# Optimization experiments

Hardware: AMD Instinct MI355X
Metric: run time of the kernel (lower is better)

The kernel has to match this reference:

```python
import jax, jax.numpy as jnp
import numpy as np

B, L, E, H = 1024, 50, 256, 256
NEG = -1e9          # stands in for -inf masked_fill (exp(NEG) == 0 in fp32)
C_EXPL = 10.0       # tanh_exploration for the pointer head
N_GLIMPSES = 1


def setup_inputs() -> dict:
    key = jax.random.key(0)
    ks = jax.random.split(key, 20)
    s = 1.0 / np.sqrt(H).astype(np.float32)
    return {
        "decoder_input": jax.random.normal(ks[0], (B, E), jnp.float32),
        "embedded_inputs": jax.random.normal(ks[1], (L, B, E), jnp.float32),
        "h0": jax.random.normal(ks[2], (B, H), jnp.float32),
        "c0": jax.random.normal(ks[3], (B, H), jnp.float32),
        "context": jax.random.normal(ks[4], (L, B, H), jnp.float32),
        "init_mask": jnp.zeros((B, L), dtype=bool),
        "lstm_Wih": jax.random.normal(ks[5], (4 * H, E), jnp.float32) * s,
        "lstm_Whh": jax.random.normal(ks[6], (4 * H, H), jnp.float32) * s,
        "lstm_bih": jax.random.normal(ks[7], (4 * H,), jnp.float32) * s,
        "lstm_bhh": jax.random.normal(ks[8], (4 * H,), jnp.float32) * s,
        "gl_Wq": jax.random.normal(ks[9], (H, H), jnp.float32) * s,
        "gl_bq": jax.random.normal(ks[10], (H,), jnp.float32) * s,
        "gl_Wref": jax.random.normal(ks[11], (H, H), jnp.float32) * s,
        "gl_bref": jax.random.normal(ks[12], (H,), jnp.float32) * s,
        "gl_v": jax.random.uniform(ks[13], (H,), jnp.float32, -s, s),
        "pt_Wq": jax.random.normal(ks[14], (H, H), jnp.float32) * s,
        "pt_bq": jax.random.normal(ks[15], (H, H // H * H,)[:1] and (H,), jnp.float32) * s,
        "pt_Wref": jax.random.normal(ks[16], (H, H), jnp.float32) * s,
        "pt_bref": jax.random.normal(ks[17], (H,), jnp.float32) * s,
        "pt_v": jax.random.uniform(ks[18], (H,), jnp.float32, -s, s),
    }


def _attention(Wq, bq, Wref, bref, v, query, context, use_tanh):
    # context: [L,B,H], query: [B,H]
    e = jnp.einsum('lbh,oh->lbo', context, Wref) + bref      # conv1d(k=1) proj of ref
    q = query @ Wq.T + bq                                    # [B,H]
    u = jnp.einsum('lbh,h->bl', jnp.tanh(q[None, :, :] + e), v)
    if use_tanh:
        u = C_EXPL * jnp.tanh(u)
    return e, u


def _lstm_cell(x, h, c, Wih, Whh, bih, bhh):
    g = x @ Wih.T + bih + h @ Whh.T + bhh
    i, f, gg, o = jnp.split(g, 4, axis=1)   # torch LSTMCell gate order: i,f,g,o
    c2 = jax.nn.sigmoid(f) * c + jax.nn.sigmoid(i) * jnp.tanh(gg)
    h2 = jax.nn.sigmoid(o) * jnp.tanh(c2)
    return h2, c2


def reference(decoder_input, embedded_inputs, h0, c0, context, init_mask,
              lstm_Wih, lstm_Whh, lstm_bih, lstm_bhh,
              gl_Wq, gl_bq, gl_Wref, gl_bref, gl_v,
              pt_Wq, pt_bq, pt_Wref, pt_bref, pt_v):
    batch_idx = jnp.arange(B)

    def step(carry, t):
        h, c, mask, idxs, dec_in = carry
        # update_mask(mask, selected), skipped at step 0 (prev_idxs is None)
        safe = jnp.maximum(idxs, 0)
        m2 = mask.at[batch_idx, safe].set(True)
        m2 = m2.at[:, -1].set(jnp.where(m2.all(axis=1), False, m2[:, -1]))
        logit_mask = jnp.where(t == 0, mask, m2)
        # LSTM cell
        hy, cy = _lstm_cell(dec_in, h, c, lstm_Wih, lstm_Whh, lstm_bih, lstm_bhh)
        g_l = hy
        # glimpse attention(s) (mask_glimpses=True)
        for _ in range(N_GLIMPSES):
            e, gl = _attention(gl_Wq, gl_bq, gl_Wref, gl_bref, gl_v, g_l, context, False)
            gl = jnp.where(logit_mask, NEG, gl)
            g_l = jnp.einsum('lbh,bl->bh', e, jax.nn.softmax(gl, axis=1))
        # pointer attention (mask_logits=True)
        _, logits = _attention(pt_Wq, pt_bq, pt_Wref, pt_bref, pt_v, g_l, context, True)
        logits = jnp.where(logit_mask, NEG, logits)
        log_p = jax.nn.log_softmax(logits, axis=1)          # [B,L]
        new_idxs = jax.lax.stop_gradient(jnp.argmax(log_p, axis=1))  # greedy decode (detached)
        new_dec_in = embedded_inputs[new_idxs, batch_idx]   # gather next input [B,E]
        return (hy, cy, logit_mask, new_idxs, new_dec_in), (log_p, new_idxs)

    init = (h0, c0, init_mask, jnp.full((B,), -1, dtype=jnp.int32), decoder_input)
    _, (log_ps, sels) = jax.lax.scan(step, init, jnp.arange(L))
    # stack along time dim 1, as torch.stack(outputs, 1)
    return jnp.transpose(log_ps, (1, 0, 2)), jnp.transpose(sels, (1, 0))
```

## Files before the change

kernel.cpp:

```cpp
#include <hip/hip_runtime.h>
#include <math.h>

#define Bsz 1024
#define Lsz 50
#define Esz 256
#define Hsz 256
#define NEGV (-1e9f)

__global__ void init_kernel(const float* __restrict__ dec0,
                            float* __restrict__ dec,
                            int* __restrict__ mask)
{
    int i = blockIdx.x * 256 + threadIdx.x;
    dec[i] = dec0[i];
    if (i < Bsz * Lsz) mask[i] = 0;
}

__global__ void transpose_wq(const float* __restrict__ WqGl, const float* __restrict__ WqPt,
                             float* __restrict__ WqGlT, float* __restrict__ WqPtT)
{
    int k = blockIdx.x;
    int n = threadIdx.x;
    if (blockIdx.y == 0) WqGlT[k * 256 + n] = WqGl[n * 256 + k];
    else                 WqPtT[k * 256 + n] = WqPt[n * 256 + k];
}

__global__ __launch_bounds__(256) void eproj_kernel(const float* __restrict__ A,
                                                    const float* __restrict__ W,
                                                    const float* __restrict__ bias,
                                                    float* __restrict__ Eo)
{
    __shared__ __align__(16) float As[16][64];
    __shared__ __align__(16) float Bs[16][64];
    const int tid = threadIdx.x;
    const int tx = tid & 15, ty = tid >> 4;
    const int ml = tid >> 2;
    const int kb = (tid & 3) << 2;
    const int m0 = blockIdx.x * 64, n0 = blockIdx.y * 64;
    const int K = Hsz;
    float acc[4][4] = {};
    for (int k0 = 0; k0 < K; k0 += 16) {
        float4 a4 = *(const float4*)(A + (size_t)(m0 + ml) * K + k0 + kb);
        float4 b4 = *(const float4*)(W + (size_t)(n0 + ml) * K + k0 + kb);
        As[kb+0][ml] = a4.x; As[kb+1][ml] = a4.y; As[kb+2][ml] = a4.z; As[kb+3][ml] = a4.w;
        Bs[kb+0][ml] = b4.x; Bs[kb+1][ml] = b4.y; Bs[kb+2][ml] = b4.z; Bs[kb+3][ml] = b4.w;
        __syncthreads();
#pragma unroll
        for (int kk = 0; kk < 16; kk++) {
            float4 av = *(const float4*)(&As[kk][ty << 2]);
            float4 bv = *(const float4*)(&Bs[kk][tx << 2]);
            float a_[4] = {av.x, av.y, av.z, av.w};
            float b_[4] = {bv.x, bv.y, bv.z, bv.w};
#pragma unroll
            for (int i = 0; i < 4; i++)
#pragma unroll
                for (int j = 0; j < 4; j++) acc[i][j] = fmaf(a_[i], b_[j], acc[i][j]);
        }
        __syncthreads();
    }
#pragma unroll
    for (int i = 0; i < 4; i++) {
        int m = m0 + (ty << 2) + i;
        int bb = m & (Bsz - 1);
        int ll = m >> 10;
#pragma unroll
        for (int j = 0; j < 4; j++) {
            int n = n0 + (tx << 2) + j;
            Eo[(size_t)bb * Lsz * Hsz + (size_t)ll * Hsz + n] = acc[i][j] + bias[n];
        }
    }
}

__global__ __launch_bounds__(256) void lstm_fused(
    const float* __restrict__ dec, const float* __restrict__ hprev,
    const float* __restrict__ cin,
    const float* __restrict__ Wih, const float* __restrict__ Whh,
    const float* __restrict__ bih, const float* __restrict__ bhh,
    float* __restrict__ hout, float* __restrict__ cout)
{
    __shared__ __align__(16) float As[16][64];
    __shared__ __align__(16) float Bs[16][64];
    const int tid = threadIdx.x;
    const int tx = tid & 15, ty = tid >> 4;
    const int ml = tid >> 2;
    const int kb = (tid & 3) << 2;
    const int m0 = blockIdx.x * 64;
    const int hh0 = blockIdx.y * 16;
    const int wrow = ((ml >> 4) << 8) + hh0 + (ml & 15);
    const int pcol = ((ml & 15) << 2) + (ml >> 4);

    float4 a4 = *(const float4*)(dec + (size_t)(m0 + ml) * 256 + kb);
    float4 b4 = *(const float4*)(Wih + (size_t)wrow * 256 + kb);

    float acc[4][4] = {};
    for (int k0 = 0; k0 < 512; k0 += 16) {
        As[kb+0][ml] = a4.x; As[kb+1][ml] = a4.y; As[kb+2][ml] = a4.z; As[kb+3][ml] = a4.w;
        Bs[kb+0][pcol] = b4.x; Bs[kb+1][pcol] = b4.y; Bs[kb+2][pcol] = b4.z; Bs[kb+3][pcol] = b4.w;
        __syncthreads();
        int k1 = k0 + 16;
        if (k1 < 512) {
            const float* A = (k1 < 256) ? dec : hprev;
            const float* W = (k1 < 256) ? Wih : Whh;
            int kk0 = k1 & 255;
            a4 = *(const float4*)(A + (size_t)(m0 + ml) * 256 + kk0 + kb);
            b4 = *(const float4*)(W + (size_t)wrow * 256 + kk0 + kb);
        }
#pragma unroll
        for (int kk = 0; kk < 16; kk++) {
            float4 av = *(const float4*)(&As[kk][ty << 2]);
            float4 bv = *(const float4*)(&Bs[kk][tx << 2]);
            float a_[4] = {av.x, av.y, av.z, av.w};
            float b_[4] = {bv.x, bv.y, bv.z, bv.w};
#pragma unroll
            for (int i = 0; i < 4; i++)
#pragma unroll
                for (int j = 0; j < 4; j++) acc[i][j] = fmaf(a_[i], b_[j], acc[i][j]);
        }
        __syncthreads();
    }

    const int hh = hh0 + tx;
    const float bi0 = bih[hh]       + bhh[hh];
    const float bf  = bih[256 + hh] + bhh[256 + hh];
    const float bg  = bih[512 + hh] + bhh[512 + hh];
    const float bo  = bih[768 + hh] + bhh[768 + hh];
#pragma unroll
    for (int i = 0; i < 4; i++) {
        int m = m0 + (ty << 2) + i;
        float gi = acc[i][0] + bi0;
        float gf = acc[i][1] + bf;
        float gc = acc[i][2] + bg;
        float go = acc[i][3] + bo;
        float ii = 1.0f / (1.0f + expf(-gi));
        float ff = 1.0f / (1.0f + expf(-gf));
        float oo = 1.0f / (1.0f + expf(-go));
        float c2 = ff * cin[(size_t)m * 256 + hh] + ii * tanhf(gc);
        hout[(size_t)m * 256 + hh] = oo * tanhf(c2);
        cout[(size_t)m * 256 + hh] = c2;
    }
}

template<bool PTR>
__global__ __launch_bounds__(256) void attn_kernel(
    const float* __restrict__ hq, const float* __restrict__ WqT,
    const float* __restrict__ bq,
    const float* __restrict__ e, const float* __restrict__ v,
    int* __restrict__ mask,
    float* __restrict__ g_out, float* __restrict__ out, int t,
    float* __restrict__ dec, const float* __restrict__ emb)
{
    __shared__ float h_s[256];
    __shared__ __align__(16) float q_s[256];
    __shared__ float u_s[64];
    __shared__ float p_s[64];
    __shared__ int sel_s;

    const int tid = threadIdx.x;
    const int lane = tid & 63, wave = tid >> 6;
    const int b = blockIdx.x;

    h_s[tid] = hq[(size_t)b * 256 + tid];
    __syncthreads();

    float q = bq[tid];
#pragma unroll 8
    for (int k = 0; k < 256; k++)
        q = fmaf(h_s[k], WqT[(size_t)k * 256 + tid], q);
    q_s[tid] = q;
    __syncthreads();

    const float4 q4 = ((const float4*)q_s)[lane];
    const float4 v4 = ((const float4*)v)[lane];
    const float* eb = e + (size_t)b * Lsz * 256;

#pragma unroll
    for (int lp = 0; lp < 13; lp++) {
        const int l = lp * 4 + wave;
        float x = 0.0f;
        if (l < Lsz) {
            float4 e4 = *(const float4*)(eb + (size_t)l * 256 + (lane << 2));
            x = v4.x * tanhf(q4.x + e4.x);
            x += v4.y * tanhf(q4.y + e4.y);
            x += v4.z * tanhf(q4.z + e4.z);
            x += v4.w * tanhf(q4.w + e4.w);
        }
#pragma unroll
        for (int o = 32; o > 0; o >>= 1) x += __shfl_xor(x, o, 64);
        if (lane == 0 && l < Lsz) u_s[l] = x;
    }
    __syncthreads();

    if (wave == 0) {
        const int l = lane;
        const int ml = (l < Lsz) ? mask[b * Lsz + l] : 0;
        float logit;
        if (l < Lsz) {
            float u = u_s[l];
            logit = PTR ? 10.0f * tanhf(u) : u;
            if (ml) logit = NEGV;
        } else logit = -1e30f;

        float m = logit;
#pragma unroll
        for (int o = 32; o > 0; o >>= 1) m = fmaxf(m, __shfl_xor(m, o, 64));
        float ex = (l < Lsz) ? expf(logit - m) : 0.0f;
        float den = ex;
#pragma unroll
        for (int o = 32; o > 0; o >>= 1) den += __shfl_xor(den, o, 64);

        if (!PTR) {
            if (l < Lsz) p_s[l] = ex / den;
        } else {
            float av = logit; int ai = (l < Lsz) ? l : 63;
#pragma unroll
            for (int o = 32; o > 0; o >>= 1) {
                float ov = __shfl_xor(av, o, 64);
                int   oi = __shfl_xor(ai, o, 64);
                if (ov > av || (ov == av && oi < ai)) { av = ov; ai = oi; }
            }
            const float lse = m + logf(den);
            if (l < Lsz)
                out[(size_t)b * Lsz * Lsz + (size_t)t * Lsz + l] = logit - lse;
            if (l == 0) {
                out[(size_t)Bsz * Lsz * Lsz + (size_t)b * Lsz + t] = (float)ai;
                sel_s = ai;
            }
            int newm = ml | (l == ai);
            unsigned long long bal = __ballot(l >= Lsz ? 1 : newm);
            int all = (bal == 0xFFFFFFFFFFFFFFFFull);
            if (l < Lsz) mask[b * Lsz + l] = (all && l == Lsz - 1) ? 0 : newm;
        }
    }
    __syncthreads();

    if (!PTR) {
        float acc = 0.0f;
        const float* ebh = eb + tid;
#pragma unroll
        for (int l = 0; l < Lsz; l++)
            acc = fmaf(p_s[l], ebh[(size_t)l * 256], acc);
        g_out[(size_t)b * 256 + tid] = acc;
    } else {
        const int s = sel_s;
        dec[(size_t)b * 256 + tid] = emb[(size_t)s * Bsz * 256 + (size_t)b * 256 + tid];
    }
}

extern "C" void kernel_launch(void* const* d_in, const int* in_sizes, int n_in,
                              void* d_out, int out_size, void* d_ws, size_t ws_size,
                              hipStream_t stream) {
    const float* decoder_input = (const float*)d_in[0];
    const float* emb           = (const float*)d_in[1];
    const float* h0            = (const float*)d_in[2];
    const float* c0            = (const float*)d_in[3];
    const float* context       = (const float*)d_in[4];
    const float* Wih    = (const float*)d_in[6];
    const float* Whh    = (const float*)d_in[7];
    const float* bih    = (const float*)d_in[8];
    const float* bhh    = (const float*)d_in[9];
    const float* glWq   = (const float*)d_in[10];
    const float* glbq   = (const float*)d_in[11];
    const float* glWref = (const float*)d_in[12];
    const float* glbref = (const float*)d_in[13];
    const float* glv    = (const float*)d_in[14];
    const float* ptWq   = (const float*)d_in[15];
    const float* ptbq   = (const float*)d_in[16];
    const float* ptWref = (const float*)d_in[17];
    const float* ptbref = (const float*)d_in[18];
    const float* ptv    = (const float*)d_in[19];

    float* out = (float*)d_out;

    float* ws    = (float*)d_ws;
    float* e_gl  = ws;
    float* e_pt  = e_gl + (size_t)Bsz * Lsz * Hsz;
    float* WqGlT = e_pt + (size_t)Bsz * Lsz * Hsz;
    float* WqPtT = WqGlT + (size_t)Hsz * Hsz;
    float* hb0   = WqPtT + (size_t)Hsz * Hsz;
    float* hb1   = hb0 + (size_t)Bsz * Hsz;
    float* cb0   = hb1 + (size_t)Bsz * Hsz;
    float* cb1   = cb0 + (size_t)Bsz * Hsz;
    float* gb    = cb1 + (size_t)Bsz * Hsz;
    float* dec   = gb  + (size_t)Bsz * Hsz;
    int*   mask  = (int*)(dec + (size_t)Bsz * Esz);

    float* hbuf[2] = {hb0, hb1};
    float* cbuf[2] = {cb0, cb1};

    init_kernel<<<dim3(Bsz), dim3(256), 0, stream>>>(decoder_input, dec, mask);
    transpose_wq<<<dim3(256, 2), dim3(256), 0, stream>>>(glWq, ptWq, WqGlT, WqPtT);

    dim3 ge(Lsz * Bsz / 64, Hsz / 64);
    eproj_kernel<<<ge, dim3(256), 0, stream>>>(context, glWref, glbref, e_gl);
    eproj_kernel<<<ge, dim3(256), 0, stream>>>(context, ptWref, ptbref, e_pt);

    for (int t = 0; t < Lsz; t++) {
        const float* hin = (t == 0) ? h0 : hbuf[(t + 1) & 1];
        const float* cin = (t == 0) ? c0 : cbuf[(t + 1) & 1];
        float* hout = hbuf[t & 1];
        float* cout = cbuf[t & 1];

        lstm_fused<<<dim3(16, 16), dim3(256), 0, stream>>>(
            dec, hin, cin, Wih, Whh, bih, bhh, hout, cout);

        attn_kernel<false><<<dim3(Bsz), dim3(256), 0, stream>>>(
            hout, WqGlT, glbq, e_gl, glv, mask, gb, nullptr, t, nullptr, nullptr);

        attn_kernel<true><<<dim3(Bsz), dim3(256), 0, stream>>>(
            gb, WqPtT, ptbq, e_pt, ptv, mask, nullptr, out, t, dec, emb);
    }
}
```

Before: 4.579 ms.

## Fuse glimpse and pointer attention into one kernel, two batch rows per block

The separate glimpse and pointer attention kernels are merged into one kernel per step. Each block now handles two batch rows, so every Wq weight load is reused for two query projections, and the glimpse result stays in shared memory instead of going through a global buffer. The shared-memory tiles in the GEMM kernels are padded from 64 to 68 columns to reduce bank conflicts, and the eproj grid is reordered so that the N-tiles of the same rows run next to each other. The cost is half as many blocks per launch (512), which lowers parallelism, and more sequential work per block.

New measurement: 5.369 ms. 17.2% more time.

```diff
diff --git a/kernel.cpp b/kernel.cpp
--- a/kernel.cpp
+++ b/kernel.cpp
@@ -30,13 +30,13 @@
                                                     const float* __restrict__ bias,
                                                     float* __restrict__ Eo)
 {
-    __shared__ __align__(16) float As[16][64];
-    __shared__ __align__(16) float Bs[16][64];
+    __shared__ __align__(16) float As[16][68];
+    __shared__ __align__(16) float Bs[16][68];
     const int tid = threadIdx.x;
     const int tx = tid & 15, ty = tid >> 4;
     const int ml = tid >> 2;
     const int kb = (tid & 3) << 2;
-    const int m0 = blockIdx.x * 64, n0 = blockIdx.y * 64;
+    const int n0 = blockIdx.x * 64, m0 = blockIdx.y * 64;
     const int K = Hsz;
     float acc[4][4] = {};
     for (int k0 = 0; k0 < K; k0 += 16) {
@@ -78,8 +78,8 @@
     const float* __restrict__ bih, const float* __restrict__ bhh,
     float* __restrict__ hout, float* __restrict__ cout)
 {
-    __shared__ __align__(16) float As[16][64];
-    __shared__ __align__(16) float Bs[16][64];
+    __shared__ __align__(16) float As[16][68];
+    __shared__ __align__(16) float Bs[16][68];
     const int tid = threadIdx.x;
     const int tx = tid & 15, ty = tid >> 4;
     const int ml = tid >> 2;
@@ -140,63 +140,132 @@
     }
 }
 
-template<bool PTR>
-__global__ __launch_bounds__(256) void attn_kernel(
-    const float* __restrict__ hq, const float* __restrict__ WqT,
-    const float* __restrict__ bq,
-    const float* __restrict__ e, const float* __restrict__ v,
-    int* __restrict__ mask,
-    float* __restrict__ g_out, float* __restrict__ out, int t,
+__global__ __launch_bounds__(256) void attn_fused(
+    const float* __restrict__ h,
+    const float* __restrict__ WqGlT, const float* __restrict__ glbq,
+    const float* __restrict__ e_gl, const float* __restrict__ glv,
+    const float* __restrict__ WqPtT, const float* __restrict__ ptbq,
+    const float* __restrict__ e_pt, const float* __restrict__ ptv,
+    int* __restrict__ mask, float* __restrict__ out, int t,
     float* __restrict__ dec, const float* __restrict__ emb)
 {
-    __shared__ float h_s[256];
-    __shared__ __align__(16) float q_s[256];
-    __shared__ float u_s[64];
-    __shared__ float p_s[64];
-    __shared__ int sel_s;
+    __shared__ float h2[2][256];
+    __shared__ __align__(16) float q_s[2][256];
+    __shared__ float g2[2][256];
+    __shared__ float u_s[2][64];
+    __shared__ float p_s[2][64];
+    __shared__ int   sel_s[2];
 
     const int tid = threadIdx.x;
     const int lane = tid & 63, wave = tid >> 6;
-    const int b = blockIdx.x;
-
-    h_s[tid] = hq[(size_t)b * 256 + tid];
-    __syncthreads();
-
-    float q = bq[tid];
+    const int b0 = blockIdx.x * 2;
+
+    h2[0][tid] = h[(size_t)b0 * 256 + tid];
+    h2[1][tid] = h[(size_t)(b0 + 1) * 256 + tid];
+    __syncthreads();
+
+    float q0 = glbq[tid], q1 = q0;
 #pragma unroll 8
-    for (int k = 0; k < 256; k++)
-        q = fmaf(h_s[k], WqT[(size_t)k * 256 + tid], q);
-    q_s[tid] = q;
-    __syncthreads();
-
-    const float4 q4 = ((const float4*)q_s)[lane];
-    const float4 v4 = ((const float4*)v)[lane];
-    const float* eb = e + (size_t)b * Lsz * 256;
-
-#pragma unroll
-    for (int lp = 0; lp < 13; lp++) {
-        const int l = lp * 4 + wave;
-        float x = 0.0f;
-        if (l < Lsz) {
-            float4 e4 = *(const float4*)(eb + (size_t)l * 256 + (lane << 2));
-            x = v4.x * tanhf(q4.x + e4.x);
-            x += v4.y * tanhf(q4.y + e4.y);
-            x += v4.z * tanhf(q4.z + e4.z);
-            x += v4.w * tanhf(q4.w + e4.w);
-        }
-#pragma unroll
-        for (int o = 32; o > 0; o >>= 1) x += __shfl_xor(x, o, 64);
-        if (lane == 0 && l < Lsz) u_s[l] = x;
-    }
-    __syncthreads();
-
-    if (wave == 0) {
-        const int l = lane;
+    for (int k = 0; k < 256; k++) {
+        float w = WqGlT[(size_t)k * 256 + tid];
+        q0 = fmaf(h2[0][k], w, q0);
+        q1 = fmaf(h2[1][k], w, q1);
+    }
+    q_s[0][tid] = q0; q_s[1][tid] = q1;
+    __syncthreads();
+
+    const float4 vg4 = ((const float4*)glv)[lane];
+
+#pragma unroll
+    for (int r = 0; r < 2; r++) {
+        const float4 q4 = ((const float4*)q_s[r])[lane];
+        const float* eb = e_gl + (size_t)(b0 + r) * Lsz * 256;
+#pragma unroll
+        for (int lp = 0; lp < 13; lp++) {
+            const int l = lp * 4 + wave;
+            float x = 0.0f;
+            if (l < Lsz) {
+                float4 e4 = *(const float4*)(eb + (size_t)l * 256 + (lane << 2));
+                x  = vg4.x * tanhf(q4.x + e4.x);
+                x += vg4.y * tanhf(q4.y + e4.y);
+                x += vg4.z * tanhf(q4.z + e4.z);
+                x += vg4.w * tanhf(q4.w + e4.w);
+            }
+#pragma unroll
+            for (int o = 32; o > 0; o >>= 1) x += __shfl_xor(x, o, 64);
+            if (lane == 0 && l < Lsz) u_s[r][l] = x;
+        }
+    }
+    __syncthreads();
+
+    if (wave < 2) {
+        const int r = wave, l = lane;
+        const int ml = (l < Lsz) ? mask[(b0 + r) * Lsz + l] : 0;
+        float logit = (l < Lsz) ? (ml ? NEGV : u_s[r][l]) : -1e30f;
+        float m = logit;
+#pragma unroll
+        for (int o = 32; o > 0; o >>= 1) m = fmaxf(m, __shfl_xor(m, o, 64));
+        float ex = (l < Lsz) ? expf(logit - m) : 0.0f;
+        float den = ex;
+#pragma unroll
+        for (int o = 32; o > 0; o >>= 1) den += __shfl_xor(den, o, 64);
+        if (l < Lsz) p_s[r][l] = ex / den;
+    }
+    __syncthreads();
+
+#pragma unroll
+    for (int r = 0; r < 2; r++) {
+        const float* ebh = e_gl + (size_t)(b0 + r) * Lsz * 256 + tid;
+        float acc = 0.0f;
+#pragma unroll
+        for (int l = 0; l < Lsz; l++)
+            acc = fmaf(p_s[r][l], ebh[(size_t)l * 256], acc);
+        g2[r][tid] = acc;
+    }
+    __syncthreads();
+
+    float p0 = ptbq[tid], p1 = p0;
+#pragma unroll 8
+    for (int k = 0; k < 256; k++) {
+        float w = WqPtT[(size_t)k * 256 + tid];
+        p0 = fmaf(g2[0][k], w, p0);
+        p1 = fmaf(g2[1][k], w, p1);
+    }
+    q_s[0][tid] = p0; q_s[1][tid] = p1;
+    __syncthreads();
+
+    const float4 vp4 = ((const float4*)ptv)[lane];
+
+#pragma unroll
+    for (int r = 0; r < 2; r++) {
+        const float4 q4 = ((const float4*)q_s[r])[lane];
+        const float* eb = e_pt + (size_t)(b0 + r) * Lsz * 256;
+#pragma unroll
+        for (int lp = 0; lp < 13; lp++) {
+            const int l = lp * 4 + wave;
+            float x = 0.0f;
+            if (l < Lsz) {
+                float4 e4 = *(const float4*)(eb + (size_t)l * 256 + (lane << 2));
+                x  = vp4.x * tanhf(q4.x + e4.x);
+                x += vp4.y * tanhf(q4.y + e4.y);
+                x += vp4.z * tanhf(q4.z + e4.z);
+                x += vp4.w * tanhf(q4.w + e4.w);
+            }
+#pragma unroll
+            for (int o = 32; o > 0; o >>= 1) x += __shfl_xor(x, o, 64);
+            if (lane == 0 && l < Lsz) u_s[r][l] = x;
+        }
+    }
+    __syncthreads();
+
+    if (wave < 2) {
+        const int r = wave, l = lane;
+        const int b = b0 + r;
         const int ml = (l < Lsz) ? mask[b * Lsz + l] : 0;
         float logit;
         if (l < Lsz) {
-            float u = u_s[l];
-            logit = PTR ? 10.0f * tanhf(u) : u;
+            float u = u_s[r][l];
+            logit = 10.0f * tanhf(u);
             if (ml) logit = NEGV;
         } else logit = -1e30f;
 
@@ -208,41 +277,32 @@
 #pragma unroll
         for (int o = 32; o > 0; o >>= 1) den += __shfl_xor(den, o, 64);
 
-        if (!PTR) {
-            if (l < Lsz) p_s[l] = ex / den;
-        } else {
-            float av = logit; int ai = (l < Lsz) ? l : 63;
-#pragma unroll
-            for (int o = 32; o > 0; o >>= 1) {
-                float ov = __shfl_xor(av, o, 64);
-                int   oi = __shfl_xor(ai, o, 64);
-                if (ov > av || (ov == av && oi < ai)) { av = ov; ai = oi; }
-            }
-            const float lse = m + logf(den);
-            if (l < Lsz)
-                out[(size_t)b * Lsz * Lsz + (size_t)t * Lsz + l] = logit - lse;
-            if (l == 0) {
-                out[(size_t)Bsz * Lsz * Lsz + (size_t)b * Lsz + t] = (float)ai;
-                sel_s = ai;
-            }
-            int newm = ml | (l == ai);
-            unsigned long long bal = __ballot(l >= Lsz ? 1 : newm);
-            int all = (bal == 0xFFFFFFFFFFFFFFFFull);
-            if (l < Lsz) mask[b * Lsz + l] = (all && l == Lsz - 1) ? 0 : newm;
-        }
-    }
-    __syncthreads();
-
-    if (!PTR) {
-        float acc = 0.0f;
-        const float* ebh = eb + tid;
-#pragma unroll
-        for (int l = 0; l < Lsz; l++)
-            acc = fmaf(p_s[l], ebh[(size_t)l * 256], acc);
-        g_out[(size_t)b * 256 + tid] = acc;
-    } else {
-        const int s = sel_s;
-        dec[(size_t)b * 256 + tid] = emb[(size_t)s * Bsz * 256 + (size_t)b * 256 + tid];
+        float av = logit; int ai = (l < Lsz) ? l : 63;
+#pragma unroll
+        for (int o = 32; o > 0; o >>= 1) {
+            float ov = __shfl_xor(av, o, 64);
+            int   oi = __shfl_xor(ai, o, 64);
+            if (ov > av || (ov == av && oi < ai)) { av = ov; ai = oi; }
+        }
+        const float lse = m + logf(den);
+        if (l < Lsz)
+            out[(size_t)b * Lsz * Lsz + (size_t)t * Lsz + l] = logit - lse;
+        if (l == 0) {
+            out[(size_t)Bsz * Lsz * Lsz + (size_t)b * Lsz + t] = (float)ai;
+            sel_s[r] = ai;
+        }
+        int newm = ml | (l == ai);
+        unsigned long long bal = __ballot(l >= Lsz ? 1 : newm);
+        int all = (bal == 0xFFFFFFFFFFFFFFFFull);
+        if (l < Lsz) mask[b * Lsz + l] = (all && l == Lsz - 1) ? 0 : newm;
+    }
+    __syncthreads();
+
+#pragma unroll
+    for (int r = 0; r < 2; r++) {
+        const int s = sel_s[r];
+        dec[(size_t)(b0 + r) * 256 + tid] =
+            emb[(size_t)s * Bsz * 256 + (size_t)(b0 + r) * 256 + tid];
     }
 }
 
@@ -280,8 +340,7 @@
     float* hb1   = hb0 + (size_t)Bsz * Hsz;
     float* cb0   = hb1 + (size_t)Bsz * Hsz;
     float* cb1   = cb0 + (size_t)Bsz * Hsz;
-    float* gb    = cb1 + (size_t)Bsz * Hsz;
-    float* dec   = gb  + (size_t)Bsz * Hsz;
+    float* dec   = cb1 + (size_t)Bsz * Hsz;
     int*   mask  = (int*)(dec + (size_t)Bsz * Esz);
 
     float* hbuf[2] = {hb0, hb1};
@@ -290,7 +349,7 @@
     init_kernel<<<dim3(Bsz), dim3(256), 0, stream>>>(decoder_input, dec, mask);
     transpose_wq<<<dim3(256, 2), dim3(256), 0, stream>>>(glWq, ptWq, WqGlT, WqPtT);
 
-    dim3 ge(Lsz * Bsz / 64, Hsz / 64);
+    dim3 ge(Hsz / 64, Lsz * Bsz / 64);
     eproj_kernel<<<ge, dim3(256), 0, stream>>>(context, glWref, glbref, e_gl);
     eproj_kernel<<<ge, dim3(256), 0, stream>>>(context, ptWref, ptbref, e_pt);
 
@@ -303,10 +362,8 @@
         lstm_fused<<<dim3(16, 16), dim3(256), 0, stream>>>(
             dec, hin, cin, Wih, Whh, bih, bhh, hout, cout);
 
-        attn_kernel<false><<<dim3(Bsz), dim3(256), 0, stream>>>(
-            hout, WqGlT, glbq, e_gl, glv, mask, gb, nullptr, t, nullptr, nullptr);
-
-        attn_kernel<true><<<dim3(Bsz), dim3(256), 0, stream>>>(
-            gb, WqPtT, ptbq, e_pt, ptv, mask, nullptr, out, t, dec, emb);
-    }
-}
+        attn_fused<<<dim3(512), dim3(256), 0, stream>>>(
+            hout, WqGlT, glbq, e_gl, glv, WqPtT, ptbq, e_pt, ptv,
+            mask, out, t, dec, emb);
+    }
+}
```

## Fuse glimpse and pointer attention into one per-row kernel; pad LDS and remap eproj tiles

Applied to the files above, without the earlier changes.

Merges the glimpse and pointer attention kernels into a single per-batch-row kernel. The glimpse vector now stays in shared memory instead of going through a global buffer, and each step needs one fewer launch. The eproj kernel gets a 1D grid with an XCD-aware tile remap so that the N-tiles of the same M-tile land on the same chiplet and share its L2. Both GEMM kernels pad their shared tiles from 64 to 68 columns to reduce bank conflicts. The fused kernel does more serial work per block, which may lengthen per-block latency.

Measured after the change: 4.383 ms. -4.3%, faster.

```diff
diff --git a/kernel.cpp b/kernel.cpp
--- a/kernel.cpp
+++ b/kernel.cpp
@@ -30,13 +30,20 @@
                                                     const float* __restrict__ bias,
                                                     float* __restrict__ Eo)
 {
-    __shared__ __align__(16) float As[16][64];
-    __shared__ __align__(16) float Bs[16][64];
+    __shared__ __align__(16) float As[16][68];
+    __shared__ __align__(16) float Bs[16][68];
     const int tid = threadIdx.x;
     const int tx = tid & 15, ty = tid >> 4;
     const int ml = tid >> 2;
     const int kb = (tid & 3) << 2;
-    const int m0 = blockIdx.x * 64, n0 = blockIdx.y * 64;
+
+    const int x = blockIdx.x;
+    const int xcd = x & 7;
+    const int j = x >> 3;
+    const int mt = xcd * 100 + (j >> 2);
+    const int nt = j & 3;
+    const int m0 = mt * 64, n0 = nt * 64;
+
     const int K = Hsz;
     float acc[4][4] = {};
     for (int k0 = 0; k0 < K; k0 += 16) {
@@ -54,7 +61,7 @@
 #pragma unroll
             for (int i = 0; i < 4; i++)
 #pragma unroll
-                for (int j = 0; j < 4; j++) acc[i][j] = fmaf(a_[i], b_[j], acc[i][j]);
+                for (int j2 = 0; j2 < 4; j2++) acc[i][j2] = fmaf(a_[i], b_[j2], acc[i][j2]);
         }
         __syncthreads();
     }
@@ -64,9 +71,9 @@
         int bb = m & (Bsz - 1);
         int ll = m >> 10;
 #pragma unroll
-        for (int j = 0; j < 4; j++) {
-            int n = n0 + (tx << 2) + j;
-            Eo[(size_t)bb * Lsz * Hsz + (size_t)ll * Hsz + n] = acc[i][j] + bias[n];
+        for (int j2 = 0; j2 < 4; j2++) {
+            int n = n0 + (tx << 2) + j2;
+            Eo[(size_t)bb * Lsz * Hsz + (size_t)ll * Hsz + n] = acc[i][j2] + bias[n];
         }
     }
 }
@@ -78,8 +85,8 @@
     const float* __restrict__ bih, const float* __restrict__ bhh,
     float* __restrict__ hout, float* __restrict__ cout)
 {
-    __shared__ __align__(16) float As[16][64];
-    __shared__ __align__(16) float Bs[16][64];
+    __shared__ __align__(16) float As[16][68];
+    __shared__ __align__(16) float Bs[16][68];
     const int tid = threadIdx.x;
     const int tx = tid & 15, ty = tid >> 4;
     const int ml = tid >> 2;
@@ -140,17 +147,18 @@
     }
 }
 
-template<bool PTR>
-__global__ __launch_bounds__(256) void attn_kernel(
-    const float* __restrict__ hq, const float* __restrict__ WqT,
-    const float* __restrict__ bq,
-    const float* __restrict__ e, const float* __restrict__ v,
-    int* __restrict__ mask,
-    float* __restrict__ g_out, float* __restrict__ out, int t,
+__global__ __launch_bounds__(256) void attn_row(
+    const float* __restrict__ h,
+    const float* __restrict__ WqGlT, const float* __restrict__ glbq,
+    const float* __restrict__ e_gl, const float* __restrict__ glv,
+    const float* __restrict__ WqPtT, const float* __restrict__ ptbq,
+    const float* __restrict__ e_pt, const float* __restrict__ ptv,
+    int* __restrict__ mask, float* __restrict__ out, int t,
     float* __restrict__ dec, const float* __restrict__ emb)
 {
     __shared__ float h_s[256];
     __shared__ __align__(16) float q_s[256];
+    __shared__ float g_s[256];
     __shared__ float u_s[64];
     __shared__ float p_s[64];
     __shared__ int sel_s;
@@ -159,34 +167,89 @@
     const int lane = tid & 63, wave = tid >> 6;
     const int b = blockIdx.x;
 
-    h_s[tid] = hq[(size_t)b * 256 + tid];
-    __syncthreads();
-
-    float q = bq[tid];
+    h_s[tid] = h[(size_t)b * 256 + tid];
+    __syncthreads();
+
+    float q = glbq[tid];
 #pragma unroll 8
     for (int k = 0; k < 256; k++)
-        q = fmaf(h_s[k], WqT[(size_t)k * 256 + tid], q);
+        q = fmaf(h_s[k], WqGlT[(size_t)k * 256 + tid], q);
     q_s[tid] = q;
     __syncthreads();
 
-    const float4 q4 = ((const float4*)q_s)[lane];
-    const float4 v4 = ((const float4*)v)[lane];
-    const float* eb = e + (size_t)b * Lsz * 256;
-
-#pragma unroll
-    for (int lp = 0; lp < 13; lp++) {
-        const int l = lp * 4 + wave;
-        float x = 0.0f;
-        if (l < Lsz) {
-            float4 e4 = *(const float4*)(eb + (size_t)l * 256 + (lane << 2));
-            x = v4.x * tanhf(q4.x + e4.x);
-            x += v4.y * tanhf(q4.y + e4.y);
-            x += v4.z * tanhf(q4.z + e4.z);
-            x += v4.w * tanhf(q4.w + e4.w);
-        }
-#pragma unroll
-        for (int o = 32; o > 0; o >>= 1) x += __shfl_xor(x, o, 64);
-        if (lane == 0 && l < Lsz) u_s[l] = x;
+    const float* ebg = e_gl + (size_t)b * Lsz * 256;
+    {
+        const float4 q4 = ((const float4*)q_s)[lane];
+        const float4 v4 = ((const float4*)glv)[lane];
+#pragma unroll
+        for (int lp = 0; lp < 13; lp++) {
+            const int l = lp * 4 + wave;
+            float x = 0.0f;
+            if (l < Lsz) {
+                float4 e4 = *(const float4*)(ebg + (size_t)l * 256 + (lane << 2));
+                x  = v4.x * tanhf(q4.x + e4.x);
+                x += v4.y * tanhf(q4.y + e4.y);
+                x += v4.z * tanhf(q4.z + e4.z);
+                x += v4.w * tanhf(q4.w + e4.w);
+            }
+#pragma unroll
+            for (int o = 32; o > 0; o >>= 1) x += __shfl_xor(x, o, 64);
+            if (lane == 0 && l < Lsz) u_s[l] = x;
+        }
+    }
+    __syncthreads();
+
+    if (wave == 0) {
+        const int l = lane;
+        const int ml = (l < Lsz) ? mask[b * Lsz + l] : 0;
+        float logit = (l < Lsz) ? (ml ? NEGV : u_s[l]) : -1e30f;
+        float m = logit;
+#pragma unroll
+        for (int o = 32; o > 0; o >>= 1) m = fmaxf(m, __shfl_xor(m, o, 64));
+        float ex = (l < Lsz) ? expf(logit - m) : 0.0f;
+        float den = ex;
+#pragma unroll
+        for (int o = 32; o > 0; o >>= 1) den += __shfl_xor(den, o, 64);
+        if (l < Lsz) p_s[l] = ex / den;
+    }
+    __syncthreads();
+
+    {
+        float acc = 0.0f;
+        const float* ebh = ebg + tid;
+#pragma unroll
+        for (int l = 0; l < Lsz; l++)
+            acc = fmaf(p_s[l], ebh[(size_t)l * 256], acc);
+        g_s[tid] = acc;
+    }
+    __syncthreads();
+
+    float p = ptbq[tid];
+#pragma unroll 8
+    for (int k = 0; k < 256; k++)
+        p = fmaf(g_s[k], WqPtT[(size_t)k * 256 + tid], p);
+    q_s[tid] = p;
+    __syncthreads();
+
+    const float* ebp = e_pt + (size_t)b * Lsz * 256;
+    {
+        const float4 q4 = ((const float4*)q_s)[lane];
+        const float4 v4 = ((const float4*)ptv)[lane];
+#pragma unroll
+        for (int lp = 0; lp < 13; lp++) {
+            const int l = lp * 4 + wave;
+            float x = 0.0f;
+            if (l < Lsz) {
+                float4 e4 = *(const float4*)(ebp + (size_t)l * 256 + (lane << 2));
+                x  = v4.x * tanhf(q4.x + e4.x);
+                x += v4.y * tanhf(q4.y + e4.y);
+                x += v4.z * tanhf(q4.z + e4.z);
+                x += v4.w * tanhf(q4.w + e4.w);
+            }
+#pragma unroll
+            for (int o = 32; o > 0; o >>= 1) x += __shfl_xor(x, o, 64);
+            if (lane == 0 && l < Lsz) u_s[l] = x;
+        }
     }
     __syncthreads();
 
@@ -196,7 +259,7 @@
         float logit;
         if (l < Lsz) {
             float u = u_s[l];
-            logit = PTR ? 10.0f * tanhf(u) : u;
+            logit = 10.0f * tanhf(u);
             if (ml) logit = NEGV;
         } else logit = -1e30f;
 
@@ -208,39 +271,28 @@
 #pragma unroll
         for (int o = 32; o > 0; o >>= 1) den += __shfl_xor(den, o, 64);
 
-        if (!PTR) {
-            if (l < Lsz) p_s[l] = ex / den;
-        } else {
-            float av = logit; int ai = (l < Lsz) ? l : 63;
-#pragma unroll
-            for (int o = 32; o > 0; o >>= 1) {
-                float ov = __shfl_xor(av, o, 64);
-                int   oi = __shfl_xor(ai, o, 64);
-                if (ov > av || (ov == av && oi < ai)) { av = ov; ai = oi; }
-            }
-            const float lse = m + logf(den);
-            if (l < Lsz)
-                out[(size_t)b * Lsz * Lsz + (size_t)t * Lsz + l] = logit - lse;
-            if (l == 0) {
-                out[(size_t)Bsz * Lsz * Lsz + (size_t)b * Lsz + t] = (float)ai;
-                sel_s = ai;
-            }
-            int newm = ml | (l == ai);
-            unsigned long long bal = __ballot(l >= Lsz ? 1 : newm);
-            int all = (bal == 0xFFFFFFFFFFFFFFFFull);
-            if (l < Lsz) mask[b * Lsz + l] = (all && l == Lsz - 1) ? 0 : newm;
-        }
-    }
-    __syncthreads();
-
-    if (!PTR) {
-        float acc = 0.0f;
-        const float* ebh = eb + tid;
-#pragma unroll
-        for (int l = 0; l < Lsz; l++)
-            acc = fmaf(p_s[l], ebh[(size_t)l * 256], acc);
-        g_out[(size_t)b * 256 + tid] = acc;
-    } else {
+        float av = logit; int ai = (l < Lsz) ? l : 63;
+#pragma unroll
+        for (int o = 32; o > 0; o >>= 1) {
+            float ov = __shfl_xor(av, o, 64);
+            int   oi = __shfl_xor(ai, o, 64);
+            if (ov > av || (ov == av && oi < ai)) { av = ov; ai = oi; }
+        }
+        const float lse = m + logf(den);
+        if (l < Lsz)
+            out[(size_t)b * Lsz * Lsz + (size_t)t * Lsz + l] = logit - lse;
+        if (l == 0) {
+            out[(size_t)Bsz * Lsz * Lsz + (size_t)b * Lsz + t] = (float)ai;
+            sel_s = ai;
+        }
+        int newm = ml | (l == ai);
+        unsigned long long bal = __ballot(l >= Lsz ? 1 : newm);
+        int all = (bal == 0xFFFFFFFFFFFFFFFFull);
+        if (l < Lsz) mask[b * Lsz + l] = (all && l == Lsz - 1) ? 0 : newm;
+    }
+    __syncthreads();
+
+    {
         const int s = sel_s;
         dec[(size_t)b * 256 + tid] = emb[(size_t)s * Bsz * 256 + (size_t)b * 256 + tid];
     }
@@ -280,8 +332,7 @@
     float* hb1   = hb0 + (size_t)Bsz * Hsz;
     float* cb0   = hb1 + (size_t)Bsz * Hsz;
     float* cb1   = cb0 + (size_t)Bsz * Hsz;
-    float* gb    = cb1 + (size_t)Bsz * Hsz;
-    float* dec   = gb  + (size_t)Bsz * Hsz;
+    float* dec   = cb1 + (size_t)Bsz * Hsz;
     int*   mask  = (int*)(dec + (size_t)Bsz * Esz);
 
     float* hbuf[2] = {hb0, hb1};
@@ -290,9 +341,8 @@
     init_kernel<<<dim3(Bsz), dim3(256), 0, stream>>>(decoder_input, dec, mask);
     transpose_wq<<<dim3(256, 2), dim3(256), 0, stream>>>(glWq, ptWq, WqGlT, WqPtT);
 
-    dim3 ge(Lsz * Bsz / 64, Hsz / 64);
-    eproj_kernel<<<ge, dim3(256), 0, stream>>>(context, glWref, glbref, e_gl);
-    eproj_kernel<<<ge, dim3(256), 0, stream>>>(context, ptWref, ptbref, e_pt);
+    eproj_kernel<<<dim3(3200), dim3(256), 0, stream>>>(context, glWref, glbref, e_gl);
+    eproj_kernel<<<dim3(3200), dim3(256), 0, stream>>>(context, ptWref, ptbref, e_pt);
 
     for (int t = 0; t < Lsz; t++) {
         const float* hin = (t == 0) ? h0 : hbuf[(t + 1) & 1];
@@ -303,10 +353,8 @@
         lstm_fused<<<dim3(16, 16), dim3(256), 0, stream>>>(
             dec, hin, cin, Wih, Whh, bih, bhh, hout, cout);
 
-        attn_kernel<false><<<dim3(Bsz), dim3(256), 0, stream>>>(
-            hout, WqGlT, glbq, e_gl, glv, mask, gb, nullptr, t, nullptr, nullptr);
-
-        attn_kernel<true><<<dim3(Bsz), dim3(256), 0, stream>>>(
-            gb, WqPtT, ptbq, e_pt, ptv, mask, nullptr, out, t, dec, emb);
-    }
-}
+        attn_row<<<dim3(Bsz), dim3(256), 0, stream>>>(
+            hout, WqGlT, glbq, e_gl, glv, WqPtT, ptbq, e_pt, ptv,
+            mask, out, t, dec, emb);
+    }
+}
```
